# Performance work log

Measured on AMD Instinct MI355X. Metric: run time of the kernel, lower is better.

Reference implementation:

```python
import jax, jax.numpy as jnp
import numpy as np
import math

# static config
NH, HD, HID = 16, 128, 2048
ROT = 64            # head_dim * partial_rotary_factor(0.5)
EPS = 1e-6
GROUPS = 8
CHUNK = 64
THETA = 10000.0
LAYER_IDX, N_LAYERS = 1, 32
B, S = 2, 2048


def _base_slopes(n):
    # power-of-two branch of HF ALiBi slopes
    start = 2 ** (-(2 ** (-(math.log2(n) - 3))))
    return [start * (start ** i) for i in range(n)]

# per-head log-decay (negative): slope = -base * (1 - (l-1)/(L-1) + 1e-5)
SLOPE = jnp.asarray(
    -np.array(_base_slopes(NH), dtype=np.float32)
    * (1.0 - (LAYER_IDX - 1) / (N_LAYERS - 1) + 1e-5),
    dtype=jnp.float32)  # [NH]


def _rmsnorm(x, w):
    return x * jax.lax.rsqrt(jnp.mean(x * x, axis=-1, keepdims=True) + EPS) * w


def _partial_rope(x, positions):
    # x: [B,S,NH,HD]; neox-style rotary on first ROT dims, rest passthrough
    half = ROT // 2
    inv_freq = 1.0 / (THETA ** (jnp.arange(half, dtype=jnp.float32) / half))
    ang = positions.astype(jnp.float32)[:, None] * inv_freq       # [S, half]
    cos = jnp.cos(ang)[None, :, None, :]
    sin = jnp.sin(ang)[None, :, None, :]
    x1, x2, rest = x[..., :half], x[..., half:ROT], x[..., ROT:]
    return jnp.concatenate(
        [x1 * cos - x2 * sin, x2 * cos + x1 * sin, rest], axis=-1)


def setup_inputs() -> dict:
    key = jax.random.key(0)
    ks = jax.random.split(key, 4)
    return {
        'positions': jnp.arange(S, dtype=jnp.int32),
        'hidden_states': jax.random.normal(ks[0], (B, S, HID), jnp.float32),
        'recurrent_state': jnp.zeros((B, NH, HD, HD), jnp.float32),
        'w_qkv': jax.random.normal(ks[1], (HID, 3 * NH * HD), jnp.float32) * 0.02,
        'w_g': jax.random.normal(ks[2], (HID, NH * HD), jnp.float32) * 0.02,
        'w_dense': jax.random.normal(ks[3], (NH * HD, HID), jnp.float32) * 0.02,
        'q_norm_w': jnp.ones((HD,), jnp.float32),
        'k_norm_w': jnp.ones((HD,), jnp.float32),
        'g_norm_w': jnp.ones((NH * HD,), jnp.float32),
    }


def reference(positions, hidden_states, recurrent_state, w_qkv, w_g, w_dense,
              q_norm_w, k_norm_w, g_norm_w):
    # fused QKV projection
    qkv = hidden_states @ w_qkv                       # [B,S,3*NH*HD]
    q, k, v = jnp.split(qkv, 3, axis=-1)
    q = q.reshape(B, S, NH, HD)
    k = k.reshape(B, S, NH, HD)
    v = v.reshape(B, S, NH, HD)

    # QK RMSNorm then partial rotary
    q = _partial_rope(_rmsnorm(q, q_norm_w), positions)
    k = _partial_rope(_rmsnorm(k, k_norm_w), positions)

    # chunked ALiBi-decayed linear attention:
    #   S_t = lam * S_{t-1} + k_t v_t^T ; o_t = q_t S_t, lam = exp(slope)
    NC = S // CHUNK
    qc = q.reshape(B, NC, CHUNK, NH, HD).transpose(1, 0, 3, 2, 4)  # [NC,B,NH,C,HD]
    kc = k.reshape(B, NC, CHUNK, NH, HD).transpose(1, 0, 3, 2, 4)
    vc = v.reshape(B, NC, CHUNK, NH, HD).transpose(1, 0, 3, 2, 4)

    t = jnp.arange(CHUNK, dtype=jnp.float32)
    # intra-chunk causal decay mask lam^(i-j), i>=j: [NH,C,C]
    dec_mask = jnp.where(t[:, None] >= t[None, :],
                         jnp.exp(SLOPE[:, None, None] * (t[:, None] - t[None, :])),
                         0.0)
    q_dec = jnp.exp(SLOPE[:, None] * (t[None, :] + 1.0))            # [NH,C] lam^(i+1)
    k_dec = jnp.exp(SLOPE[:, None] * (CHUNK - 1.0 - t[None, :]))    # [NH,C] lam^(C-1-j)
    lam_C = jnp.exp(SLOPE * CHUNK)                                   # [NH]

    def step(state, inp):
        qb, kb, vb = inp                                  # [B,NH,C,HD]
        scores = jnp.einsum('bhid,bhjd->bhij', qb, kb) * dec_mask[None]
        o_intra = jnp.einsum('bhij,bhjd->bhid', scores, vb)
        o_inter = jnp.einsum('bhid,bhde->bhie', qb * q_dec[None, :, :, None], state)
        new_state = (state * lam_C[None, :, None, None]
                     + jnp.einsum('bhjd,bhje->bhde', kb * k_dec[None, :, :, None], vb))
        return new_state, o_intra + o_inter

    _, o = jax.lax.scan(step, recurrent_state, (qc, kc, vc))  # o: [NC,B,NH,C,HD]
    o = o.transpose(1, 0, 3, 2, 4).reshape(B, S, NH * HD)

    # GroupRMSNorm on attention output, sigmoid gate, output projection
    og = o.reshape(B, S, GROUPS, (NH * HD) // GROUPS)
    og = og * jax.lax.rsqrt(jnp.mean(og * og, axis=-1, keepdims=True) + EPS)
    o = og.reshape(B, S, NH * HD) * g_norm_w
    o = o * jax.nn.sigmoid(hidden_states @ w_g)
    return o @ w_dense
```

## Files before the change

kernel.cpp:

```cpp
#include <hip/hip_runtime.h>
#include <hip/hip_bf16.h>
#include <math.h>

#define NH   16
#define HD   128
#define HID  2048
#define NKV  6144
#define B_   2
#define S_   2048
#define NC   32
#define CHUNK_ 64
#define GROUPS_ 8

typedef __bf16 bf16_t;
typedef bf16_t bf16x8 __attribute__((ext_vector_type(8)));
typedef float  f32x4  __attribute__((ext_vector_type(4)));

__device__ __forceinline__ float b2f(unsigned int u) {
    union { unsigned int u; float f; } c; c.u = (u & 0xffffu) << 16; return c.f;
}
__device__ __forceinline__ unsigned int f2b(float f) {
    union { float f; unsigned int u; } c; c.f = f;
    unsigned int u = c.u;
    return (u + 0x7fffu + ((u >> 16) & 1u)) >> 16;
}

#define GLOAD_LDS16(gp, lp) __builtin_amdgcn_global_load_lds(                     \
    (const __attribute__((address_space(1))) void*)(gp),                          \
    (__attribute__((address_space(3))) void*)(lp), 16, 0, 0)

__global__ __launch_bounds__(256) void cvt_bf16(const float* __restrict__ in,
                                                unsigned short* __restrict__ out, int n8)
{
    int i = blockIdx.x * 256 + threadIdx.x;
    if (i >= n8) return;
    const float4* p = (const float4*)in + (size_t)i * 2;
    float4 a = p[0], b = p[1];
    uint4 o;
    o.x = f2b(a.x) | (f2b(a.y) << 16);
    o.y = f2b(a.z) | (f2b(a.w) << 16);
    o.z = f2b(b.x) | (f2b(b.y) << 16);
    o.w = f2b(b.z) | (f2b(b.w) << 16);
    ((uint4*)out)[i] = o;
}

__global__ __launch_bounds__(256) void transpose_cvt(const float* __restrict__ in,
                                                     unsigned short* __restrict__ out,
                                                     int Kdim, int Ndim)
{
    __shared__ float tile[32][33];
    int ntx = Ndim >> 5;
    int bx = blockIdx.x % ntx;
    int by = blockIdx.x / ntx;
    int lx = threadIdx.x & 31, ly = threadIdx.x >> 5;
    int r0 = by * 32, c0 = bx * 32;
    #pragma unroll
    for (int r = 0; r < 4; ++r)
        tile[ly + r * 8][lx] = in[(size_t)(r0 + ly + r * 8) * Ndim + c0 + lx];
    __syncthreads();
    #pragma unroll
    for (int r = 0; r < 4; ++r)
        out[(size_t)(c0 + ly + r * 8) * Kdim + r0 + lx] = (unsigned short)f2b(tile[lx][ly + r * 8]);
}

__device__ __forceinline__ void storeOne(float* p, float v) { *p = v; }
__device__ __forceinline__ void storeOne(unsigned short* p, float v) { *p = (unsigned short)f2b(v); }

template <typename OutT>
__global__ __launch_bounds__(256) void gemm_mfma(const bf16_t* __restrict__ A,
                                                 const bf16_t* __restrict__ Bt,
                                                 OutT* __restrict__ C,
                                                 int M, int N, int K)
{
    __shared__ bf16_t As[128 * 32];
    __shared__ bf16_t Bs[128 * 32];
    int tid  = threadIdx.x;
    int ntiles = N >> 7;
    int bx = blockIdx.x % ntiles;
    int by = blockIdx.x / ntiles;
    int lane = tid & 63;
    int wave = tid >> 6;
    int wm = (wave >> 1) * 64;
    int wn = (wave & 1) * 64;
    int l16  = lane & 15;
    int quad = lane >> 4;

    f32x4 acc[4][4];
    #pragma unroll
    for (int i = 0; i < 4; ++i)
        #pragma unroll
        for (int j = 0; j < 4; ++j) { f32x4 z = {0.f, 0.f, 0.f, 0.f}; acc[i][j] = z; }

    const bf16_t* aG = A  + (size_t)(by * 128 + (tid >> 2)) * K + (tid & 3) * 8;
    const bf16_t* bG = Bt + (size_t)(bx * 128 + (tid >> 2)) * K + (tid & 3) * 8;
    bf16_t* aL0 = As + tid * 8;
    bf16_t* aL1 = As + 2048 + tid * 8;
    bf16_t* bL0 = Bs + tid * 8;
    bf16_t* bL1 = Bs + 2048 + tid * 8;
    const size_t half = (size_t)64 * K;

    for (int kt = 0; kt < K; kt += 32) {
        GLOAD_LDS16(aG + kt,        aL0);
        GLOAD_LDS16(aG + half + kt, aL1);
        GLOAD_LDS16(bG + kt,        bL0);
        GLOAD_LDS16(bG + half + kt, bL1);
        __syncthreads();
        bf16x8 af[4], bf[4];
        #pragma unroll
        for (int t = 0; t < 4; ++t) {
            af[t] = *(const bf16x8*)(As + (wm + t * 16 + l16) * 32 + quad * 8);
            bf[t] = *(const bf16x8*)(Bs + (wn + t * 16 + l16) * 32 + quad * 8);
        }
        #pragma unroll
        for (int mt = 0; mt < 4; ++mt)
            #pragma unroll
            for (int nt = 0; nt < 4; ++nt)
                acc[mt][nt] = __builtin_amdgcn_mfma_f32_16x16x32_bf16(af[mt], bf[nt], acc[mt][nt], 0, 0, 0);
        __syncthreads();
    }

    #pragma unroll
    for (int mt = 0; mt < 4; ++mt)
        #pragma unroll
        for (int nt = 0; nt < 4; ++nt) {
            int col = bx * 128 + wn + nt * 16 + l16;
            #pragma unroll
            for (int r = 0; r < 4; ++r) {
                int row = by * 128 + wm + mt * 16 + quad * 4 + r;
                storeOne(C + (size_t)row * N + col, acc[mt][nt][r]);
            }
        }
}


__device__ __forceinline__ void ld_fr4(bf16x8 (&d)[4][2], const bf16_t* b, int s0, int ri) {
    #pragma unroll
    for (int i = 0; i < 4; ++i)
        #pragma unroll
        for (int k = 0; k < 2; ++k)
            d[i][k] = *(const bf16x8*)(b + (((s0 + i) * 2 + k) << 9) + ri);
}
__device__ __forceinline__ void ld_fr2(bf16x8 (&d)[2][2], const bf16_t* b, int s0, int ri) {
    #pragma unroll
    for (int i = 0; i < 2; ++i)
        #pragma unroll
        for (int k = 0; k < 2; ++k)
            d[i][k] = *(const bf16x8*)(b + (((s0 + i) * 2 + k) << 9) + ri);
}
__device__ __forceinline__ void mfma_quad(f32x4 (&a)[4][2], const bf16x8 (&af)[4][2],
                                          const bf16x8 (&bv)[2][2]) {
    #pragma unroll
    for (int mt = 0; mt < 4; ++mt)
        #pragma unroll
        for (int nt = 0; nt < 2; ++nt)
            #pragma unroll
            for (int ks = 0; ks < 2; ++ks)
                a[mt][nt] = __builtin_amdgcn_mfma_f32_16x16x32_bf16(af[mt][ks], bv[nt][ks], a[mt][nt], 0, 0, 0);
}

#define PH_PRE()  do { asm volatile("s_barrier" ::: "memory");                    \
                       asm volatile("s_waitcnt lgkmcnt(0)" ::: "memory");         \
                       __builtin_amdgcn_sched_barrier(0);                         \
                       __builtin_amdgcn_s_setprio(1); } while (0)
#define PH_POST() do { __builtin_amdgcn_s_setprio(0);                             \
                       asm volatile("s_barrier" ::: "memory"); } while (0)
#define VMCNT6()  asm volatile("s_waitcnt vmcnt(6)" ::: "memory")
#define VMCNT4()  asm volatile("s_waitcnt vmcnt(4)" ::: "memory")
#define VMCNT0()  asm volatile("s_waitcnt vmcnt(0)" ::: "memory")

__global__ __launch_bounds__(512, 2) void gemm_qg_256(const bf16_t* __restrict__ A,
                                                      const bf16_t* __restrict__ Bt,
                                                      unsigned short* __restrict__ Cq,
                                                      unsigned short* __restrict__ Cg)
{
    __shared__ bf16_t Asm[2][2][8192];
    __shared__ bf16_t Bsm[2][2][8192];
    const int K  = HID;
    const int NT = K / 64;

    int tid  = threadIdx.x;
    int wave = tid >> 6, lane = tid & 63;
    int wm = wave >> 2, wn = wave & 3;
    int l16 = lane & 15, quad = lane >> 4;
    int wm4 = wm * 4, wn2 = wn * 2;

    int bid = blockIdx.x;
    int wg  = (bid & 7) * 64 + (bid >> 3);
    int bx  = wg & 31;
    int by  = wg >> 5;

    int rd_in = ((l16 << 5) | (quad << 3)) ^ (((l16 >> 3) & 1) << 4);

    int ch = lane ^ ((lane & 32) >> 4);
    int rr = ch >> 2;
    int cc = (ch & 3) * 8;

    const bf16_t* aSrc0 = A  + (size_t)(by * 256 +       wave * 16 + rr) * K + cc;
    const bf16_t* aSrc1 = A  + (size_t)(by * 256 + 128 + wave * 16 + rr) * K + cc;
    const bf16_t* bSrc0 = Bt + (size_t)(bx * 256 +       wave * 16 + rr) * K + cc;
    const bf16_t* bSrc1 = Bt + (size_t)(bx * 256 + 128 + wave * 16 + rr) * K + cc;

#define STAGE_A(h, t) do {                                                        \
        const bf16_t* _g = ((h) ? aSrc1 : aSrc0) + (size_t)(t) * 64;              \
        bf16_t* _l = &Asm[(t) & 1][(h)][wave * 1024 + lane * 8];                  \
        GLOAD_LDS16(_g,      _l);                                                 \
        GLOAD_LDS16(_g + 32, _l + 512); } while (0)
#define STAGE_B(h, t) do {                                                        \
        const bf16_t* _g = ((h) ? bSrc1 : bSrc0) + (size_t)(t) * 64;              \
        bf16_t* _l = &Bsm[(t) & 1][(h)][wave * 1024 + lane * 8];                  \
        GLOAD_LDS16(_g,      _l);                                                 \
        GLOAD_LDS16(_g + 32, _l + 512); } while (0)

    f32x4 acc[2][2][4][2];
    #pragma unroll
    for (int a0 = 0; a0 < 2; ++a0)
        #pragma unroll
        for (int a1 = 0; a1 < 2; ++a1)
            #pragma unroll
            for (int a2 = 0; a2 < 4; ++a2)
                #pragma unroll
                for (int a3 = 0; a3 < 2; ++a3) { f32x4 z = {0.f,0.f,0.f,0.f}; acc[a0][a1][a2][a3] = z; }
    bf16x8 af[4][2], bfv[2][2];

    STAGE_A(0, 0); STAGE_B(1, 0); STAGE_A(1, 0); STAGE_B(0, 0);
    VMCNT4();
    STAGE_A(0, 1); STAGE_B(1, 1); STAGE_A(1, 1);
    VMCNT6();
    asm volatile("s_barrier" ::: "memory");

    #pragma unroll 2
    for (int t = 0; t < NT - 2; ++t) {
        int buf = t & 1;
        ld_fr4(af,  &Asm[buf][0][0], wm4, rd_in);
        ld_fr2(bfv, &Bsm[buf][0][0], wn2, rd_in);
        STAGE_B(0, t + 1);
        PH_PRE(); mfma_quad(acc[0][0], af, bfv); PH_POST();
        ld_fr2(bfv, &Bsm[buf][1][0], wn2, rd_in);
        STAGE_A(0, t + 2);
        PH_PRE(); mfma_quad(acc[0][1], af, bfv); PH_POST();
        ld_fr4(af,  &Asm[buf][1][0], wm4, rd_in);
        STAGE_B(1, t + 2);
        PH_PRE(); mfma_quad(acc[1][1], af, bfv); PH_POST();
        ld_fr2(bfv, &Bsm[buf][0][0], wn2, rd_in);
        STAGE_A(1, t + 2);
        VMCNT6();
        PH_PRE(); mfma_quad(acc[1][0], af, bfv); PH_POST();
    }
    {
        const int buf = (NT - 2) & 1;
        ld_fr4(af,  &Asm[buf][0][0], wm4, rd_in);
        ld_fr2(bfv, &Bsm[buf][0][0], wn2, rd_in);
        STAGE_B(0, NT - 1);
        PH_PRE(); mfma_quad(acc[0][0], af, bfv); PH_POST();
        ld_fr2(bfv, &Bsm[buf][1][0], wn2, rd_in);
        PH_PRE(); mfma_quad(acc[0][1], af, bfv); PH_POST();
        ld_fr4(af,  &Asm[buf][1][0], wm4, rd_in);
        PH_PRE(); mfma_quad(acc[1][1], af, bfv); PH_POST();
        ld_fr2(bfv, &Bsm[buf][0][0], wn2, rd_in);
        VMCNT0();
        PH_PRE(); mfma_quad(acc[1][0], af, bfv); PH_POST();
    }
    {
        const int buf = (NT - 1) & 1;
        ld_fr4(af,  &Asm[buf][0][0], wm4, rd_in);
        ld_fr2(bfv, &Bsm[buf][0][0], wn2, rd_in);
        PH_PRE(); mfma_quad(acc[0][0], af, bfv); PH_POST();
        ld_fr2(bfv, &Bsm[buf][1][0], wn2, rd_in);
        PH_PRE(); mfma_quad(acc[0][1], af, bfv); PH_POST();
        ld_fr4(af,  &Asm[buf][1][0], wm4, rd_in);
        PH_PRE(); mfma_quad(acc[1][1], af, bfv); PH_POST();
        ld_fr2(bfv, &Bsm[buf][0][0], wn2, rd_in);
        PH_PRE(); mfma_quad(acc[1][0], af, bfv); PH_POST();
    }
#undef STAGE_A
#undef STAGE_B

    unsigned short* Cc; int Nn, colbase;
    if (bx < 24) { Cc = Cq; Nn = NKV; colbase = bx * 256; }
    else         { Cc = Cg; Nn = HID; colbase = bx * 256 - NKV; }
    int row0 = by * 256 + wm * 64 + quad * 4;
    int col0 = colbase + wn * 32 + l16;
    #pragma unroll
    for (int mh = 0; mh < 2; ++mh)
        #pragma unroll
        for (int nh = 0; nh < 2; ++nh)
            #pragma unroll
            for (int mt = 0; mt < 4; ++mt)
                #pragma unroll
                for (int nt = 0; nt < 2; ++nt) {
                    int col = col0 + nh * 128 + nt * 16;
                    #pragma unroll
                    for (int r = 0; r < 4; ++r) {
                        int row = row0 + mh * 128 + mt * 16 + r;
                        Cc[(size_t)row * Nn + col] = (unsigned short)f2b(acc[mh][nh][mt][nt][r]);
                    }
                }
}

__global__ __launch_bounds__(256) void norm_rope(unsigned short* __restrict__ qkv,
                                                 const int* __restrict__ positions,
                                                 const float* __restrict__ qw,
                                                 const float* __restrict__ kw)
{
    int bs = blockIdx.x;
    int s  = bs & (S_ - 1);
    int tid = threadIdx.x;
    int l16 = tid & 15;
    unsigned short* base = qkv + (size_t)bs * NKV;
    float pos = (float)positions[s];

    #pragma unroll
    for (int p = 0; p < 2; ++p) {
        int rr = p * 16 + (tid >> 4);
        int qk = rr >> 4;
        int h  = rr & 15;
        unsigned short* row = base + qk * HID + h * HD;
        const float* w = qk ? kw : qw;
        uint4 v = *(const uint4*)(row + l16 * 8);
        float x[8];
        x[0] = b2f(v.x); x[1] = b2f(v.x >> 16);
        x[2] = b2f(v.y); x[3] = b2f(v.y >> 16);
        x[4] = b2f(v.z); x[5] = b2f(v.z >> 16);
        x[6] = b2f(v.w); x[7] = b2f(v.w >> 16);
        float ss = 0.f;
        #pragma unroll
        for (int t = 0; t < 8; ++t) ss += x[t] * x[t];
        ss += __shfl_xor(ss, 1); ss += __shfl_xor(ss, 2);
        ss += __shfl_xor(ss, 4); ss += __shfl_xor(ss, 8);
        float inv = rsqrtf(ss * (1.0f / 128.0f) + 1e-6f);
        float n[8];
        #pragma unroll
        for (int t = 0; t < 8; ++t) n[t] = x[t] * inv * w[l16 * 8 + t];
        float pr[8];
        #pragma unroll
        for (int t = 0; t < 8; ++t) pr[t] = __shfl_xor(n[t], 4);
        if (l16 < 8) {
            #pragma unroll
            for (int t = 0; t < 8; ++t) {
                int dim = l16 * 8 + t;
                int i = dim & 31;
                float ang = pos * exp2f(-(float)i * 0.4152410118609203f);
                float cs = cosf(ang), sn = sinf(ang);
                n[t] = (dim < 32) ? (n[t] * cs - pr[t] * sn) : (n[t] * cs + pr[t] * sn);
            }
        }
        uint4 o;
        o.x = f2b(n[0]) | (f2b(n[1]) << 16);
        o.y = f2b(n[2]) | (f2b(n[3]) << 16);
        o.z = f2b(n[4]) | (f2b(n[5]) << 16);
        o.w = f2b(n[6]) | (f2b(n[7]) << 16);
        *(uint4*)(row + l16 * 8) = o;
    }
}

__global__ __launch_bounds__(256) void chunk_kv(const unsigned short* __restrict__ qkv,
                                                unsigned short* __restrict__ wbuf)
{
    __shared__ unsigned short kt[128 * 72];
    __shared__ unsigned short vt[128 * 72];
    int bi = blockIdx.x;
    int c = bi & 31, bh = bi >> 5, h = bh & 15, b = bh >> 4;
    int tid = threadIdx.x;
    float slope = -exp2f(-0.5f * (float)(h + 1)) * (1.0f + 1e-5f);

    const unsigned short* kbase = qkv + ((size_t)(b * S_ + c * CHUNK_)) * NKV + HID + h * HD;
    const unsigned short* vbase = kbase + HID;

    for (int idx = tid; idx < 4096; idx += 256) {
        int j = idx >> 6, p = idx & 63;
        unsigned int ku = *(const unsigned int*)(kbase + (size_t)j * NKV + p * 2);
        kt[(2 * p) * 72 + j]     = (unsigned short)(ku & 0xffffu);
        kt[(2 * p + 1) * 72 + j] = (unsigned short)(ku >> 16);
        float kd = expf(slope * (float)(63 - j));
        unsigned int vu = *(const unsigned int*)(vbase + (size_t)j * NKV + p * 2);
        vt[(2 * p) * 72 + j]     = (unsigned short)f2b(b2f(vu) * kd);
        vt[(2 * p + 1) * 72 + j] = (unsigned short)f2b(b2f(vu >> 16) * kd);
    }
    __syncthreads();

    int lane = tid & 63, wave = tid >> 6;
    int wm = (wave >> 1) * 64;
    int wn = (wave & 1) * 64;
    int l16 = lane & 15, quad = lane >> 4;

    f32x4 acc[4][4];
    #pragma unroll
    for (int i = 0; i < 4; ++i)
        #pragma unroll
        for (int j = 0; j < 4; ++j) { f32x4 z = {0.f,0.f,0.f,0.f}; acc[i][j] = z; }

    #pragma unroll
    for (int ks = 0; ks < 64; ks += 32) {
        bf16x8 af[4], bf[4];
        #pragma unroll
        for (int t = 0; t < 4; ++t) {
            af[t] = *(const bf16x8*)((const bf16_t*)vt + (wm + t * 16 + l16) * 72 + ks + quad * 8);
            bf[t] = *(const bf16x8*)((const bf16_t*)kt + (wn + t * 16 + l16) * 72 + ks + quad * 8);
        }
        #pragma unroll
        for (int mt = 0; mt < 4; ++mt)
            #pragma unroll
            for (int nt = 0; nt < 4; ++nt)
                acc[mt][nt] = __builtin_amdgcn_mfma_f32_16x16x32_bf16(af[mt], bf[nt], acc[mt][nt], 0, 0, 0);
    }

    unsigned short* wp = wbuf + ((size_t)bi << 14);
    #pragma unroll
    for (int mt = 0; mt < 4; ++mt)
        #pragma unroll
        for (int nt = 0; nt < 4; ++nt) {
            int dcol = wn + nt * 16 + l16;
            #pragma unroll
            for (int r = 0; r < 4; ++r) {
                int erow = wm + mt * 16 + quad * 4 + r;
                wp[(size_t)erow * 128 + dcol] = (unsigned short)f2b(acc[mt][nt][r]);
            }
        }
}

__global__ __launch_bounds__(256) void state_scan(const unsigned short* __restrict__ wbuf,
                                                  const float* __restrict__ rs0,
                                                  unsigned short* __restrict__ stbuf)
{
    int bi = blockIdx.x;
    int es = bi & 15, bh = bi >> 4, h = bh & 15, b = bh >> 4;
    int tid = threadIdx.x;
    float slope = -exp2f(-0.5f * (float)(h + 1)) * (1.0f + 1e-5f);
    float lam = expf(slope * 64.0f);

    int e  = es * 8 + (tid >> 5);
    int d0 = (tid & 31) * 4;

    float S[4];
    const float* rp = rs0 + ((size_t)(b * NH + h)) * HD * HD + e;
    #pragma unroll
    for (int t = 0; t < 4; ++t) S[t] = rp[(size_t)(d0 + t) * HD];

    size_t off = (size_t)e * 128 + d0;
    for (int c = 0; c < NC; ++c) {
        size_t base = (((size_t)bh * NC + c) << 14) + off;
        uint2 o;
        o.x = f2b(S[0]) | (f2b(S[1]) << 16);
        o.y = f2b(S[2]) | (f2b(S[3]) << 16);
        *(uint2*)(stbuf + base) = o;
        uint2 w = *(const uint2*)(wbuf + base);
        S[0] = S[0] * lam + b2f(w.x);
        S[1] = S[1] * lam + b2f(w.x >> 16);
        S[2] = S[2] * lam + b2f(w.y);
        S[3] = S[3] * lam + b2f(w.y >> 16);
    }
}

__global__ __launch_bounds__(256) void chunk_out(const unsigned short* __restrict__ qkv,
                                                 const unsigned short* __restrict__ stbuf,
                                                 unsigned short* __restrict__ obuf)
{
    __shared__ unsigned short qs[64 * 136];
    __shared__ unsigned short vt[128 * 72];
    __shared__ unsigned short sc[64 * 72];

    int bi = blockIdx.x;
    int c = bi & 31, bh = bi >> 5, h = bh & 15, b = bh >> 4;
    int tid = threadIdx.x;
    float slope = -exp2f(-0.5f * (float)(h + 1)) * (1.0f + 1e-5f);

    int lane = tid & 63, wave = tid >> 6;
    int l16 = lane & 15, quad = lane >> 4;
    int wn3 = wave * 32;

    const unsigned short* stp = stbuf + (((size_t)bh * NC + c) << 14);
    bf16x8 bsf[4][2];
    #pragma unroll
    for (int ksp4 = 0; ksp4 < 4; ++ksp4)
        #pragma unroll
        for (int nt = 0; nt < 2; ++nt)
            bsf[ksp4][nt] = *(const bf16x8*)((const bf16_t*)stp +
                (size_t)(wn3 + nt * 16 + l16) * 128 + ksp4 * 32 + quad * 8);

    const unsigned short* qrow = qkv + ((size_t)(b * S_ + c * CHUNK_)) * NKV + h * HD;
    const unsigned short* krow = qrow + HID;
    for (int idx = tid; idx < 1024; idx += 256) {
        int row = idx >> 4, c8 = (idx & 15) * 8;
        *(uint4*)(qs + row * 136 + c8) = *(const uint4*)(qrow + (size_t)row * NKV + c8);
    }
    const unsigned short* vbase = qrow + 2 * HID;
    for (int idx = tid; idx < 4096; idx += 256) {
        int j = idx >> 6, p = idx & 63;
        unsigned int vu = *(const unsigned int*)(vbase + (size_t)j * NKV + p * 2);
        vt[(2 * p) * 72 + j]     = (unsigned short)(vu & 0xffffu);
        vt[(2 * p + 1) * 72 + j] = (unsigned short)(vu >> 16);
    }
    __syncthreads();

    {
        f32x4 accS[4];
        #pragma unroll
        for (int t = 0; t < 4; ++t) { f32x4 z = {0.f,0.f,0.f,0.f}; accS[t] = z; }
        #pragma unroll
        for (int ksp = 0; ksp < 128; ksp += 32) {
            bf16x8 aq = *(const bf16x8*)((const bf16_t*)qs + (wave * 16 + l16) * 136 + ksp + quad * 8);
            #pragma unroll
            for (int nt = 0; nt < 4; ++nt) {
                bf16x8 bk = *(const bf16x8*)((const bf16_t*)krow + (size_t)(nt * 16 + l16) * NKV + ksp + quad * 8);
                accS[nt] = __builtin_amdgcn_mfma_f32_16x16x32_bf16(aq, bk, accS[nt], 0, 0, 0);
            }
        }
        float ad[4];
        #pragma unroll
        for (int r = 0; r < 4; ++r) ad[r] = expf(slope * (float)(wave * 16 + quad * 4 + r));
        #pragma unroll
        for (int nt = 0; nt < 4; ++nt) {
            int j = nt * 16 + l16;
            float bd = expf(-slope * (float)j);
            #pragma unroll
            for (int r = 0; r < 4; ++r) {
                int i = wave * 16 + quad * 4 + r;
                float v = (i >= j) ? accS[nt][r] * ad[r] * bd : 0.0f;
                sc[i * 72 + j] = (unsigned short)f2b(v);
            }
        }
    }
    __syncthreads();

    f32x4 accI[4][2], accE[4][2];
    #pragma unroll
    for (int i = 0; i < 4; ++i)
        #pragma unroll
        for (int j = 0; j < 2; ++j) { f32x4 z = {0.f,0.f,0.f,0.f}; accI[i][j] = z; accE[i][j] = z; }

    #pragma unroll
    for (int ksp = 0; ksp < 64; ksp += 32) {
        bf16x8 as[4], bv[2];
        #pragma unroll
        for (int mt = 0; mt < 4; ++mt)
            as[mt] = *(const bf16x8*)((const bf16_t*)sc + (mt * 16 + l16) * 72 + ksp + quad * 8);
        #pragma unroll
        for (int nt = 0; nt < 2; ++nt)
            bv[nt] = *(const bf16x8*)((const bf16_t*)vt + (wn3 + nt * 16 + l16) * 72 + ksp + quad * 8);
        #pragma unroll
        for (int mt = 0; mt < 4; ++mt)
            #pragma unroll
            for (int nt = 0; nt < 2; ++nt)
                accI[mt][nt] = __builtin_amdgcn_mfma_f32_16x16x32_bf16(as[mt], bv[nt], accI[mt][nt], 0, 0, 0);
    }
    #pragma unroll
    for (int ksp4 = 0; ksp4 < 4; ++ksp4) {
        bf16x8 aq[4];
        #pragma unroll
        for (int mt = 0; mt < 4; ++mt)
            aq[mt] = *(const bf16x8*)((const bf16_t*)qs + (mt * 16 + l16) * 136 + ksp4 * 32 + quad * 8);
        #pragma unroll
        for (int mt = 0; mt < 4; ++mt)
            #pragma unroll
            for (int nt = 0; nt < 2; ++nt)
                accE[mt][nt] = __builtin_amdgcn_mfma_f32_16x16x32_bf16(aq[mt], bsf[ksp4][nt], accE[mt][nt], 0, 0, 0);
    }

    #pragma unroll
    for (int mt = 0; mt < 4; ++mt) {
        #pragma unroll
        for (int r = 0; r < 4; ++r) {
            int i = mt * 16 + quad * 4 + r;
            float qd = expf(slope * (float)(i + 1));
            int orow = b * S_ + c * CHUNK_ + i;
            #pragma unroll
            for (int nt = 0; nt < 2; ++nt) {
                int col = h * HD + wn3 + nt * 16 + l16;
                float o = accI[mt][nt][r] + qd * accE[mt][nt][r];
                obuf[(size_t)orow * 2048 + col] = (unsigned short)f2b(o);
            }
        }
    }
}

__global__ __launch_bounds__(256) void gnorm_gate(const unsigned short* __restrict__ o,
                                                  unsigned short* __restrict__ gate,
                                                  const float* __restrict__ gw)
{
    int row = blockIdx.x >> 3;
    int g   = blockIdx.x & 7;
    int col = g * 256 + threadIdx.x;
    size_t idx = (size_t)row * 2048 + col;
    float ov = b2f(o[idx]);
    float ss = ov * ov;
    #pragma unroll
    for (int off = 32; off > 0; off >>= 1) ss += __shfl_xor(ss, off);
    __shared__ float part[4];
    if ((threadIdx.x & 63) == 0) part[threadIdx.x >> 6] = ss;
    __syncthreads();
    float tot = part[0] + part[1] + part[2] + part[3];
    float inv = rsqrtf(tot * (1.0f / 256.0f) + 1e-6f);
    float gv = b2f(gate[idx]);
    float sig = 1.0f / (1.0f + expf(-gv));
    gate[idx] = (unsigned short)f2b(ov * inv * gw[col] * sig);
}

extern "C" void kernel_launch(void* const* d_in, const int* in_sizes, int n_in,
                              void* d_out, int out_size, void* d_ws, size_t ws_size,
                              hipStream_t stream) {
    const int*   positions = (const int*)d_in[0];
    const float* hidden    = (const float*)d_in[1];
    const float* rstate    = (const float*)d_in[2];
    const float* w_qkv     = (const float*)d_in[3];
    const float* w_g       = (const float*)d_in[4];
    const float* w_dense   = (const float*)d_in[5];
    const float* q_norm_w  = (const float*)d_in[6];
    const float* k_norm_w  = (const float*)d_in[7];
    const float* g_norm_w  = (const float*)d_in[8];
    float* out = (float*)d_out;

    const int MR = B_ * S_;

    char* w = (char*)d_ws;
    unsigned short* qkv  = (unsigned short*)w;            w += (size_t)MR * NKV * 2;
    unsigned short* gbuf = (unsigned short*)w;            w += (size_t)MR * 2048 * 2;
    unsigned short* wdT  = (unsigned short*)w;            w += (size_t)HID * HID * 2;
    char* regionA = w;                                    w += (size_t)MR * HID * 2 + (size_t)8192 * HID * 2;
    char* regionB = w;
    unsigned short* hbf   = (unsigned short*)regionA;
    unsigned short* btQG  = (unsigned short*)(regionA + (size_t)MR * HID * 2);
    unsigned short* wqT   = btQG;
    unsigned short* wgT   = btQG + (size_t)NKV * HID;
    unsigned short* stbuf = (unsigned short*)regionA;
    unsigned short* wbuf  = (unsigned short*)regionB;
    unsigned short* obuf  = (unsigned short*)regionB;

    cvt_bf16<<<dim3((MR * HID / 8 + 255) / 256), dim3(256), 0, stream>>>(hidden, hbf, MR * HID / 8);
    transpose_cvt<<<dim3((HID / 32) * (NKV / 32)), dim3(256), 0, stream>>>(w_qkv, wqT, HID, NKV);
    transpose_cvt<<<dim3((HID / 32) * (HID / 32)), dim3(256), 0, stream>>>(w_g, wgT, HID, HID);
    transpose_cvt<<<dim3((HID / 32) * (HID / 32)), dim3(256), 0, stream>>>(w_dense, wdT, HID, HID);

    gemm_qg_256<<<dim3(512), dim3(512), 0, stream>>>(
        (const bf16_t*)hbf, (const bf16_t*)btQG, qkv, gbuf);
    norm_rope<<<dim3(B_ * S_), dim3(256), 0, stream>>>(qkv, positions, q_norm_w, k_norm_w);

    chunk_kv<<<dim3(B_ * NH * NC), dim3(256), 0, stream>>>(qkv, wbuf);
    state_scan<<<dim3(B_ * NH * 16), dim3(256), 0, stream>>>(wbuf, rstate, stbuf);
    chunk_out<<<dim3(B_ * NH * NC), dim3(256), 0, stream>>>(qkv, stbuf, obuf);

    gnorm_gate<<<dim3(MR * GROUPS_), dim3(256), 0, stream>>>(obuf, gbuf, g_norm_w);
    gemm_mfma<float><<<dim3((MR / 128) * (HID / 128)), dim3(256), 0, stream>>>(
        (const bf16_t*)gbuf, (const bf16_t*)wdT, out, MR, HID, HID);
}
```

Measured before the change: 487.1 us.

## Double-buffer MFMA fragments across phases and regroup workgroups per XCD

Restructures the main loop of the QKV/gate GEMM so LDS fragment loads for the next phase and the next K-tile are issued before the current MFMA phase, using separate A/B fragment registers (afA/afB, bf0/bf1). It drops the explicit lgkmcnt(0) waits and reduces barrier pairs so LDS reads overlap matrix math. It also changes the block-to-tile mapping so each XCD gets a contiguous 8x8 tile region, aiming for better L2 reuse. The extra fragment registers raise register pressure, and the looser waits rely on compiler-inserted waitcnts for correctness.

```diff
diff --git a/kernel.cpp b/kernel.cpp
--- a/kernel.cpp
+++ b/kernel.cpp
@@ -158,14 +158,11 @@
                 a[mt][nt] = __builtin_amdgcn_mfma_f32_16x16x32_bf16(af[mt][ks], bv[nt][ks], a[mt][nt], 0, 0, 0);
 }
 
-#define PH_PRE()  do { asm volatile("s_barrier" ::: "memory");                    \
-                       asm volatile("s_waitcnt lgkmcnt(0)" ::: "memory");         \
-                       __builtin_amdgcn_sched_barrier(0);                         \
-                       __builtin_amdgcn_s_setprio(1); } while (0)
-#define PH_POST() do { __builtin_amdgcn_s_setprio(0);                             \
-                       asm volatile("s_barrier" ::: "memory"); } while (0)
+#define BAR()     asm volatile("s_barrier" ::: "memory")
+#define PRIO1()   __builtin_amdgcn_s_setprio(1)
+#define PRIO0()   __builtin_amdgcn_s_setprio(0)
+#define SCHEDB()  __builtin_amdgcn_sched_barrier(0)
 #define VMCNT6()  asm volatile("s_waitcnt vmcnt(6)" ::: "memory")
-#define VMCNT4()  asm volatile("s_waitcnt vmcnt(4)" ::: "memory")
 #define VMCNT0()  asm volatile("s_waitcnt vmcnt(0)" ::: "memory")
 
 __global__ __launch_bounds__(512, 2) void gemm_qg_256(const bf16_t* __restrict__ A,
@@ -185,9 +182,9 @@
     int wm4 = wm * 4, wn2 = wn * 2;
 
     int bid = blockIdx.x;
-    int wg  = (bid & 7) * 64 + (bid >> 3);
-    int bx  = wg & 31;
-    int by  = wg >> 5;
+    int xcd = bid & 7, idx = bid >> 3;
+    int by  = (xcd >> 2) * 8 + (idx >> 3);
+    int bx  = (xcd & 3) * 8 + (idx & 7);
 
     int rd_in = ((l16 << 5) | (quad << 3)) ^ (((l16 >> 3) & 1) << 4);
 
@@ -220,57 +217,74 @@
             for (int a2 = 0; a2 < 4; ++a2)
                 #pragma unroll
                 for (int a3 = 0; a3 < 2; ++a3) { f32x4 z = {0.f,0.f,0.f,0.f}; acc[a0][a1][a2][a3] = z; }
-    bf16x8 af[4][2], bfv[2][2];
-
-    STAGE_A(0, 0); STAGE_B(1, 0); STAGE_A(1, 0); STAGE_B(0, 0);
-    VMCNT4();
+
+    bf16x8 afA[4][2], afB[4][2];
+    bf16x8 bf0[2][2], bf1[2][2];
+
+    STAGE_A(0, 0); STAGE_B(0, 0); STAGE_B(1, 0); STAGE_A(1, 0);
     STAGE_A(0, 1); STAGE_B(1, 1); STAGE_A(1, 1);
     VMCNT6();
-    asm volatile("s_barrier" ::: "memory");
+    BAR();
+    ld_fr4(afA, &Asm[0][0][0], wm4, rd_in);
+    ld_fr2(bf1, &Bsm[0][1][0], wn2, rd_in);
+    ld_fr2(bf0, &Bsm[0][0][0], wn2, rd_in);
 
     #pragma unroll 2
     for (int t = 0; t < NT - 2; ++t) {
-        int buf = t & 1;
-        ld_fr4(af,  &Asm[buf][0][0], wm4, rd_in);
-        ld_fr2(bfv, &Bsm[buf][0][0], wn2, rd_in);
+        const int buf = t & 1, nbuf = buf ^ 1;
         STAGE_B(0, t + 1);
-        PH_PRE(); mfma_quad(acc[0][0], af, bfv); PH_POST();
-        ld_fr2(bfv, &Bsm[buf][1][0], wn2, rd_in);
+        BAR();
+        PRIO1(); mfma_quad(acc[0][0], afA, bf0); PRIO0();
+        BAR();
+        ld_fr4(afB, &Asm[buf][1][0], wm4, rd_in);
         STAGE_A(0, t + 2);
-        PH_PRE(); mfma_quad(acc[0][1], af, bfv); PH_POST();
-        ld_fr4(af,  &Asm[buf][1][0], wm4, rd_in);
+        SCHEDB();
+        BAR();
+        PRIO1(); mfma_quad(acc[0][1], afA, bf1); PRIO0();
+        BAR();
         STAGE_B(1, t + 2);
-        PH_PRE(); mfma_quad(acc[1][1], af, bfv); PH_POST();
-        ld_fr2(bfv, &Bsm[buf][0][0], wn2, rd_in);
+        BAR();
+        PRIO1(); mfma_quad(acc[1][1], afB, bf1); PRIO0();
+        BAR();
         STAGE_A(1, t + 2);
         VMCNT6();
-        PH_PRE(); mfma_quad(acc[1][0], af, bfv); PH_POST();
+        BAR();
+        ld_fr4(afA, &Asm[nbuf][0][0], wm4, rd_in);
+        ld_fr2(bf1, &Bsm[nbuf][1][0], wn2, rd_in);
+        SCHEDB();
+        PRIO1(); mfma_quad(acc[1][0], afB, bf0); PRIO0();
+        ld_fr2(bf0, &Bsm[nbuf][0][0], wn2, rd_in);
+        BAR();
     }
     {
-        const int buf = (NT - 2) & 1;
-        ld_fr4(af,  &Asm[buf][0][0], wm4, rd_in);
-        ld_fr2(bfv, &Bsm[buf][0][0], wn2, rd_in);
-        STAGE_B(0, NT - 1);
-        PH_PRE(); mfma_quad(acc[0][0], af, bfv); PH_POST();
-        ld_fr2(bfv, &Bsm[buf][1][0], wn2, rd_in);
-        PH_PRE(); mfma_quad(acc[0][1], af, bfv); PH_POST();
-        ld_fr4(af,  &Asm[buf][1][0], wm4, rd_in);
-        PH_PRE(); mfma_quad(acc[1][1], af, bfv); PH_POST();
-        ld_fr2(bfv, &Bsm[buf][0][0], wn2, rd_in);
+        const int t = NT - 2, buf = t & 1, nbuf = buf ^ 1;
+        STAGE_B(0, t + 1);
+        BAR();
+        PRIO1(); mfma_quad(acc[0][0], afA, bf0); PRIO0();
+        BAR();
+        ld_fr4(afB, &Asm[buf][1][0], wm4, rd_in);
+        SCHEDB();
+        BAR();
+        PRIO1(); mfma_quad(acc[0][1], afA, bf1); PRIO0();
+        BAR();
+        PRIO1(); mfma_quad(acc[1][1], afB, bf1); PRIO0();
         VMCNT0();
-        PH_PRE(); mfma_quad(acc[1][0], af, bfv); PH_POST();
+        BAR();
+        ld_fr4(afA, &Asm[nbuf][0][0], wm4, rd_in);
+        ld_fr2(bf1, &Bsm[nbuf][1][0], wn2, rd_in);
+        SCHEDB();
+        PRIO1(); mfma_quad(acc[1][0], afB, bf0); PRIO0();
+        ld_fr2(bf0, &Bsm[nbuf][0][0], wn2, rd_in);
+        BAR();
     }
     {
         const int buf = (NT - 1) & 1;
-        ld_fr4(af,  &Asm[buf][0][0], wm4, rd_in);
-        ld_fr2(bfv, &Bsm[buf][0][0], wn2, rd_in);
-        PH_PRE(); mfma_quad(acc[0][0], af, bfv); PH_POST();
-        ld_fr2(bfv, &Bsm[buf][1][0], wn2, rd_in);
-        PH_PRE(); mfma_quad(acc[0][1], af, bfv); PH_POST();
-        ld_fr4(af,  &Asm[buf][1][0], wm4, rd_in);
-        PH_PRE(); mfma_quad(acc[1][1], af, bfv); PH_POST();
-        ld_fr2(bfv, &Bsm[buf][0][0], wn2, rd_in);
-        PH_PRE(); mfma_quad(acc[1][0], af, bfv); PH_POST();
+        PRIO1(); mfma_quad(acc[0][0], afA, bf0); PRIO0();
+        ld_fr4(afB, &Asm[buf][1][0], wm4, rd_in);
+        SCHEDB();
+        PRIO1(); mfma_quad(acc[0][1], afA, bf1); PRIO0();
+        PRIO1(); mfma_quad(acc[1][1], afB, bf1); PRIO0();
+        PRIO1(); mfma_quad(acc[1][0], afB, bf0); PRIO0();
     }
 #undef STAGE_A
 #undef STAGE_B
```

New measurement: 464.7 us. 1.05x faster.
